# Optimization experiments

Measured on AMD Instinct MI355X. Metric: run time of the kernel, lower is better.

Reference implementation:

```python
import jax, jax.numpy as jnp
import numpy as np

N, E, F, H, D, B = 50000, 800000, 128, 4, 32, 8  # nodes, edges, feat, heads, head_dim, graphs
NEG_SLOPE = 0.2


def _layer_norm(x, g, b, eps=1e-5):
    mu = jnp.mean(x, axis=-1, keepdims=True)
    var = jnp.var(x, axis=-1, keepdims=True)
    return (x - mu) * jax.lax.rsqrt(var + eps) * g + b


def _gat(x, src, dst, W, a_src, a_dst, bias):
    # PyG GATConv (eval): linear -> per-node alpha terms -> edge logits ->
    # per-destination segment softmax -> scatter-add weighted messages.
    h = (x @ W).reshape(N, H, D)                                  # [N,H,D]
    al_s = jnp.einsum('nhd,hd->nh', h, a_src)                     # [N,H]
    al_d = jnp.einsum('nhd,hd->nh', h, a_dst)                     # [N,H]
    logits = jax.nn.leaky_relu(al_s[src] + al_d[dst], NEG_SLOPE)  # [E+N,H]
    m = jax.ops.segment_max(logits, dst, num_segments=N)          # [N,H]
    ex = jnp.exp(logits - m[dst])
    denom = jax.ops.segment_sum(ex, dst, num_segments=N)          # [N,H]
    alpha = ex / denom[dst]                                       # [E+N,H]
    msg = h[src] * alpha[..., None]                               # [E+N,H,D]
    out = jax.ops.segment_sum(msg, dst, num_segments=N)           # [N,H,D]
    return out.reshape(N, H * D) + bias


def _gat_block(x, src, dst, W, a_src, a_dst, bias, ln_g, ln_b):
    out = _gat(x, src, dst, W, a_src, a_dst, bias)
    return _layer_norm(out + x, ln_g, ln_b)  # residual: dims match (128==128)


def setup_inputs() -> dict:
    key = jax.random.key(0)
    ks = jax.random.split(key, 24)
    s = 0.05
    inp = {
        'x': jax.random.normal(ks[0], (N, F), jnp.float32),
        'edge_index': jax.random.randint(ks[1], (2, E), 0, N, jnp.int32),
        'batch': jnp.sort(jax.random.randint(ks[2], (N,), 0, B, jnp.int32)),
    }
    i = 3
    for p in ('loc', 'reg'):
        inp[p + '_W'] = jax.random.normal(ks[i], (F, H * D)) * s; i += 1
        inp[p + '_att_src'] = jax.random.normal(ks[i], (H, D)) * s; i += 1
        inp[p + '_att_dst'] = jax.random.normal(ks[i], (H, D)) * s; i += 1
        inp[p + '_bias'] = jnp.zeros((H * D,))
        inp[p + '_ln_g'] = jnp.ones((F,))
        inp[p + '_ln_b'] = jnp.zeros((F,))
    inp['gp_W1'] = jax.random.normal(ks[i], (F, F)) * s; i += 1
    inp['gp_b1'] = jnp.zeros((F,))
    inp['gp_W2'] = jax.random.normal(ks[i], (F, F)) * s; i += 1
    inp['gp_b2'] = jnp.zeros((F,))
    inp['fu_W1'] = jax.random.normal(ks[i], (3 * F, 2 * F)) * s; i += 1
    inp['fu_b1'] = jnp.zeros((2 * F,))
    inp['fu_W2'] = jax.random.normal(ks[i], (2 * F, F)) * s; i += 1
    inp['fu_b2'] = jnp.zeros((F,))
    inp['fu_ln_g'] = jnp.ones((F,))
    inp['fu_ln_b'] = jnp.zeros((F,))
    return inp


def reference(x, edge_index, batch,
              loc_W, loc_att_src, loc_att_dst, loc_bias, loc_ln_g, loc_ln_b,
              reg_W, reg_att_src, reg_att_dst, reg_bias, reg_ln_g, reg_ln_b,
              gp_W1, gp_b1, gp_W2, gp_b2,
              fu_W1, fu_b1, fu_W2, fu_b2, fu_ln_g, fu_ln_b):
    # add self-loops (PyG GATConv default add_self_loops=True)
    loops = jnp.arange(N, dtype=edge_index.dtype)
    src = jnp.concatenate([edge_index[0], loops])
    dst = jnp.concatenate([edge_index[1], loops])

    local = _gat_block(x, src, dst, loc_W, loc_att_src, loc_att_dst, loc_bias, loc_ln_g, loc_ln_b)
    regional = _gat_block(x, src, dst, reg_W, reg_att_src, reg_att_dst, reg_bias, reg_ln_g, reg_ln_b)

    # global mean pool per graph, broadcast back to nodes
    sums = jax.ops.segment_sum(x, batch, num_segments=B)                  # [B,F]
    cnts = jax.ops.segment_sum(jnp.ones((N, 1), x.dtype), batch, num_segments=B)
    gctx = (sums / cnts)[batch]                                           # [N,F]
    gfeat = jax.nn.relu(gctx @ gp_W1 + gp_b1) @ gp_W2 + gp_b2

    cat = jnp.concatenate([local, regional, gfeat], axis=-1)              # [N,3F]
    fused = jax.nn.relu(cat @ fu_W1 + fu_b1) @ fu_W2 + fu_b2
    return _layer_norm(fused, fu_ln_g, fu_ln_b)
```

## Files before the change

kernel.cpp:

```cpp
#include <hip/hip_runtime.h>

#define NN 50000
#define EE 800000
#define FF 128
#define HH 4
#define BB 8
#define NEG 0.2f
#define NBLK ((NN + 255) / 256)

typedef __attribute__((ext_vector_type(8))) short s8v;
typedef __attribute__((ext_vector_type(4))) float f4v;

__device__ __forceinline__ unsigned short f2b(float f) {
    union { float f; unsigned u; } v; v.f = f;
    unsigned r = v.u + 0x7fffu + ((v.u >> 16) & 1u);
    return (unsigned short)(r >> 16);
}
__device__ __forceinline__ float b2f(unsigned short h) {
    union { unsigned u; float f; } v; v.u = ((unsigned)h) << 16;
    return v.f;
}
__device__ __forceinline__ float uasf(unsigned u) {
    union { unsigned u; float f; } v; v.u = u; return v.f;
}
__device__ __forceinline__ float lrelu(float t) { return t > 0.f ? t : NEG * t; }

__global__ void k_init(int* cur, float* pooled) {
    int i = blockIdx.x * 256 + threadIdx.x;
    if (i < NN) cur[i] = 1;
    if (i < BB * FF) pooled[i] = 0.f;
}

__global__ void k_count(const int* __restrict__ ei, int* cur) {
    int i = blockIdx.x * 256 + threadIdx.x;
    if (i < EE) atomicAdd(&cur[ei[EE + i]], 1);
}

__global__ __launch_bounds__(256) void k_scanA(int* cur, int* row_ptr, int* bsum) {
    __shared__ int wsum[4];
    int b = blockIdx.x, t = threadIdx.x;
    int i = b * 256 + t;
    int v = (i < NN) ? cur[i] : 0;
    if (i < NN) cur[i] = 0;
    int lane = t & 63, w = t >> 6;
    int sc = v;
#pragma unroll
    for (int off = 1; off < 64; off <<= 1) {
        int n = __shfl_up(sc, off);
        if (lane >= off) sc += n;
    }
    if (lane == 63) wsum[w] = sc;
    __syncthreads();
    int woff = 0;
    for (int k = 0; k < w; k++) woff += wsum[k];
    int incl = sc + woff;
    if (i < NN) row_ptr[i + 1] = incl;
    if (t == 255) bsum[b] = incl;
    if (i == 0) row_ptr[0] = 0;
}

__global__ __launch_bounds__(256) void k_scanB(const int* __restrict__ bsum, int* boff) {
    __shared__ int wsum[4];
    int t = threadIdx.x;
    int v = (t < NBLK) ? bsum[t] : 0;
    int lane = t & 63, w = t >> 6;
    int sc = v;
#pragma unroll
    for (int off = 1; off < 64; off <<= 1) {
        int n = __shfl_up(sc, off);
        if (lane >= off) sc += n;
    }
    if (lane == 63) wsum[w] = sc;
    __syncthreads();
    int woff = 0;
    for (int k = 0; k < w; k++) woff += wsum[k];
    if (t < NBLK) boff[t] = sc + woff - v;
}

__global__ __launch_bounds__(256) void k_scanC(int* row_ptr, const int* __restrict__ boff) {
    int i = blockIdx.x * 256 + threadIdx.x;
    if (i < NN) row_ptr[i + 1] += boff[blockIdx.x];
}

__global__ void k_scatter(const int* __restrict__ ei, const int* __restrict__ row_ptr,
                          int* cur, int* col) {
    int i = blockIdx.x * 256 + threadIdx.x;
    if (i < EE) {
        int s = ei[i], d = ei[EE + i];
        int p = atomicAdd(&cur[d], 1);
        col[row_ptr[d] + p] = s;
    } else if (i < EE + NN) {
        int n = i - EE;
        int p = atomicAdd(&cur[n], 1);
        col[row_ptr[n] + p] = n;
    }
}

__global__ void k_convw(const float* __restrict__ locW, const float* __restrict__ regW,
                        const float* __restrict__ W1, const float* __restrict__ W2,
                        unsigned short* __restrict__ Wt, unsigned short* __restrict__ W1t,
                        unsigned short* __restrict__ W2t) {
    int i = blockIdx.x * 256 + threadIdx.x;
    if (i < 32768) {
        int n = i >> 7, k = i & 127;
        float v = n < 128 ? locW[k * 128 + n] : regW[k * 128 + n - 128];
        Wt[i] = f2b(v);
    } else if (i < 32768 + 98304) {
        int j = i - 32768; int n = j / 384, k = j - n * 384;
        W1t[j] = f2b(W1[k * 256 + n]);
    } else if (i < 163840) {
        int j = i - 131072; int n = j >> 8, k = j & 255;
        W2t[j] = f2b(W2[k * 128 + n]);
    }
}

__global__ __launch_bounds__(256) void k_gemm1(
    const float* __restrict__ x,
    const unsigned short* __restrict__ Wt,
    const float* __restrict__ loc_as, const float* __restrict__ loc_ad,
    const float* __restrict__ reg_as, const float* __restrict__ reg_ad,
    unsigned* __restrict__ hc,
    float* __restrict__ als_l, float* __restrict__ ald_l,
    float* __restrict__ als_r, float* __restrict__ ald_r) {
    __shared__ unsigned short As[4 * 64 * 8];
    __shared__ unsigned short Bs[4 * 256 * 8];
    __shared__ unsigned short Hs[32 * 64 * 8];
    int t = threadIdx.x;
    int w = t >> 6, l = t & 63;
    int lq = l >> 4, lr = l & 15;
    int r0 = blockIdx.x * 64;

    int srow = t >> 2, sg = t & 3;
    int snode = r0 + srow; if (snode >= NN) snode = NN - 1;
    const float* xrow = x + (size_t)snode * 128 + sg * 8;

    f4v acc[4][4];
#pragma unroll
    for (int a0 = 0; a0 < 4; a0++)
#pragma unroll
        for (int b0 = 0; b0 < 4; b0++) acc[a0][b0] = (f4v){0.f, 0.f, 0.f, 0.f};

    for (int ks = 0; ks < 4; ++ks) {
        {
            float4 f0 = *(const float4*)(xrow + ks * 32);
            float4 f1 = *(const float4*)(xrow + ks * 32 + 4);
            unsigned short u[8] = { f2b(f0.x), f2b(f0.y), f2b(f0.z), f2b(f0.w),
                                    f2b(f1.x), f2b(f1.y), f2b(f1.z), f2b(f1.w) };
            *(s8v*)&As[(sg * 64 + srow) * 8] = *(const s8v*)u;
        }
#pragma unroll
        for (int it = 0; it < 4; ++it) {
            int c = t + it * 256;
            int g = c & 3, n = c >> 2;
            *(s8v*)&Bs[(g * 256 + n) * 8] = *(const s8v*)&Wt[(size_t)n * 128 + ks * 32 + g * 8];
        }
        __syncthreads();
        s8v af[4], bf[4];
#pragma unroll
        for (int rf = 0; rf < 4; ++rf) af[rf] = *(const s8v*)&As[(lq * 64 + rf * 16 + lr) * 8];
#pragma unroll
        for (int cf = 0; cf < 4; ++cf) bf[cf] = *(const s8v*)&Bs[(lq * 256 + w * 64 + cf * 16 + lr) * 8];
#pragma unroll
        for (int rf = 0; rf < 4; ++rf)
#pragma unroll
            for (int cf = 0; cf < 4; ++cf)
                acc[rf][cf] = __builtin_amdgcn_mfma_f32_16x16x32_bf16(af[rf], bf[cf], acc[rf][cf], 0, 0, 0);
        __syncthreads();
    }
#pragma unroll
    for (int cf = 0; cf < 4; ++cf) {
        int c = w * 64 + cf * 16 + lr;
#pragma unroll
        for (int rf = 0; rf < 4; ++rf)
#pragma unroll
            for (int i = 0; i < 4; ++i) {
                int row = rf * 16 + lq * 4 + i;
                Hs[((c >> 3) * 64 + row) * 8 + (c & 7)] = f2b(acc[rf][cf][i]);
            }
    }
    __syncthreads();
#pragma unroll
    for (int it = 0; it < 16; ++it) {
        int idx = t + it * 256;
        int row = idx >> 6, fp = idx & 63;
        int node = r0 + row;
        if (node < NN) {
            int c0 = 2 * fp;
            int c1 = 128 + 2 * fp;
            unsigned lo = *(const unsigned*)&Hs[((c0 >> 3) * 64 + row) * 8 + (c0 & 7)];
            unsigned hi = *(const unsigned*)&Hs[((c1 >> 3) * 64 + row) * 8 + (c1 & 7)];
            uint2 p; p.x = lo; p.y = hi;
            *(uint2*)&hc[(size_t)node * 128 + fp * 2] = p;
        }
    }
#pragma unroll
    for (int it = 0; it < 4; ++it) {
        int row = it * 16 + (t >> 4);
        int node = r0 + row;
        int q = t & 15;
        int gat = q >> 3, sd = (q >> 2) & 1, head = q & 3;
        const float* av = gat ? (sd ? reg_ad : reg_as) : (sd ? loc_ad : loc_as);
        float s = 0.f;
        int cbase = gat * 128 + head * 32;
        for (int d = 0; d < 32; ++d) {
            int c = cbase + d;
            s += b2f(Hs[((c >> 3) * 64 + row) * 8 + (c & 7)]) * av[head * 32 + d];
        }
        if (node < NN) {
            float* outp = gat ? (sd ? ald_r : als_r) : (sd ? ald_l : als_l);
            outp[(size_t)node * 4 + head] = s;
        }
    }
}

__global__ void k_pool(const float* __restrict__ x, const int* __restrict__ batch,
                       float* pooled) {
    int t = threadIdx.x;
    int f = t & 127, half = t >> 7;
    int rstart = blockIdx.x * 256;
    int rend = rstart + 256; if (rend > NN) rend = NN;
    float acc = 0.f; int cur_b = -1;
    for (int r = rstart + half; r < rend; r += 2) {
        int b = batch[r];
        if (b != cur_b) {
            if (cur_b >= 0) atomicAdd(&pooled[cur_b * 128 + f], acc);
            cur_b = b; acc = 0.f;
        }
        acc += x[r * 128 + f];
    }
    if (cur_b >= 0) atomicAdd(&pooled[cur_b * 128 + f], acc);
}

__global__ __launch_bounds__(256) void k_gfeat8(
    const float* __restrict__ pooled, const int* __restrict__ batch,
    const float* __restrict__ W1, const float* __restrict__ b1,
    const float* __restrict__ W2, const float* __restrict__ b2,
    unsigned short* __restrict__ g8b) {
    __shared__ float mean_s[128];
    __shared__ float hid_s[128];
    __shared__ float part[256];
    __shared__ int bnd[2];
    int b = blockIdx.x, t = threadIdx.x;
    if (t < 2) {
        int target = b + t;
        int lo = 0, hi = NN;
        while (lo < hi) { int mid = (lo + hi) >> 1; if (batch[mid] < target) lo = mid + 1; else hi = mid; }
        bnd[t] = lo;
    }
    __syncthreads();
    int cnt = bnd[1] - bnd[0];
    float inv = cnt ? 1.f / (float)cnt : 0.f;
    if (t < 128) mean_s[t] = pooled[b * 128 + t] * inv;
    __syncthreads();
    int c = t & 127, kh = t >> 7;
    float a = 0.f;
    for (int k = kh * 64; k < kh * 64 + 64; k++) a += mean_s[k] * W1[k * 128 + c];
    part[t] = a;
    __syncthreads();
    if (t < 128) hid_s[t] = fmaxf(part[t] + part[t + 128] + b1[t], 0.f);
    __syncthreads();
    float a2 = 0.f;
    for (int k = kh * 64; k < kh * 64 + 64; k++) a2 += hid_s[k] * W2[k * 128 + c];
    part[t] = a2;
    __syncthreads();
    if (t < 128) g8b[b * 128 + t] = f2b(part[t] + part[t + 128] + b2[t]);
}

__global__ __launch_bounds__(256) void k_gat(
    const int* __restrict__ row_ptr, const int* __restrict__ col,
    const unsigned* __restrict__ hc,
    const float* __restrict__ als_l, const float* __restrict__ ald_l,
    const float* __restrict__ als_r, const float* __restrict__ ald_r,
    const float* __restrict__ x,
    const float* __restrict__ loc_bias, const float* __restrict__ loc_g, const float* __restrict__ loc_b,
    const float* __restrict__ reg_bias, const float* __restrict__ reg_g, const float* __restrict__ reg_b,
    unsigned short* __restrict__ out_local, unsigned short* __restrict__ out_reg) {
    __shared__ float exA[4][64][4];
    __shared__ float exB[4][64][4];
    __shared__ int   colb[4][64];
    __shared__ int   degs[4];
    int w = threadIdx.x >> 6, lane = threadIdx.x & 63;
    int hA = lane >> 4;
    int node = blockIdx.x * 4 + w;
    int rp0 = row_ptr[node];
    int deg = row_ptr[node + 1] - rp0;
    if (lane == 0) degs[w] = deg;
    float4 adL = *(const float4*)&ald_l[(size_t)node * 4];
    float4 adR = *(const float4*)&ald_r[(size_t)node * 4];
    __syncthreads();
    int maxdeg = max(max(degs[0], degs[1]), max(degs[2], degs[3]));
    int chunks = (maxdeg + 63) >> 6;

    float sL0 = 0.f, sL1 = 0.f, sL2 = 0.f, sL3 = 0.f;
    float sR0 = 0.f, sR1 = 0.f, sR2 = 0.f, sR3 = 0.f;
    for (int base = 0; base < deg; base += 64) {
        int i = base + lane;
        bool v = i < deg;
        int s = col[rp0 + (v ? i : deg - 1)];
        float4 aL = *(const float4*)&als_l[(size_t)s * 4];
        float4 aR = *(const float4*)&als_r[(size_t)s * 4];
        float e0 = __expf(lrelu(aL.x + adL.x));
        float e1 = __expf(lrelu(aL.y + adL.y));
        float e2 = __expf(lrelu(aL.z + adL.z));
        float e3 = __expf(lrelu(aL.w + adL.w));
        float f0 = __expf(lrelu(aR.x + adR.x));
        float f1 = __expf(lrelu(aR.y + adR.y));
        float f2 = __expf(lrelu(aR.z + adR.z));
        float f3 = __expf(lrelu(aR.w + adR.w));
        if (!v) { e0 = e1 = e2 = e3 = f0 = f1 = f2 = f3 = 0.f; }
        *(float4*)&exA[w][lane][0] = make_float4(e0, e1, e2, e3);
        *(float4*)&exB[w][lane][0] = make_float4(f0, f1, f2, f3);
        colb[w][lane] = s;
        sL0 += e0; sL1 += e1; sL2 += e2; sL3 += e3;
        sR0 += f0; sR1 += f1; sR2 += f2; sR3 += f3;
    }
    __syncthreads();
#pragma unroll
    for (int off = 32; off; off >>= 1) {
        sL0 += __shfl_xor(sL0, off); sL1 += __shfl_xor(sL1, off);
        sL2 += __shfl_xor(sL2, off); sL3 += __shfl_xor(sL3, off);
        sR0 += __shfl_xor(sR0, off); sR1 += __shfl_xor(sR1, off);
        sR2 += __shfl_xor(sR2, off); sR3 += __shfl_xor(sR3, off);
    }
    float iA = (hA & 2) ? ((hA & 1) ? 1.f / sL3 : 1.f / sL2)
                        : ((hA & 1) ? 1.f / sL1 : 1.f / sL0);
    float iB = (hA & 2) ? ((hA & 1) ? 1.f / sR3 : 1.f / sR2)
                        : ((hA & 1) ? 1.f / sR1 : 1.f / sR0);

    float a0 = 0.f, a1 = 0.f, b0 = 0.f, b1 = 0.f;
    const uint2* hcp = (const uint2*)hc;
    if (chunks == 1) {
#pragma unroll 4
        for (int e = 0; e < deg; ++e) {
            int s = colb[w][e];
            float eAv = exA[w][e][hA];
            float eBv = exB[w][e][hA];
            uint2 u = hcp[(size_t)s * 64 + lane];
            a0 += eAv * uasf(u.x << 16);
            a1 += eAv * uasf(u.x & 0xffff0000u);
            b0 += eBv * uasf(u.y << 16);
            b1 += eBv * uasf(u.y & 0xffff0000u);
        }
    } else {
        for (int c = 0; c < chunks; ++c) {
            int base = c * 64, i = base + lane;
            if (i < deg) {
                int s = col[rp0 + i];
                float4 aL = *(const float4*)&als_l[(size_t)s * 4];
                float4 aR = *(const float4*)&als_r[(size_t)s * 4];
                *(float4*)&exA[w][lane][0] = make_float4(
                    __expf(lrelu(aL.x + adL.x)), __expf(lrelu(aL.y + adL.y)),
                    __expf(lrelu(aL.z + adL.z)), __expf(lrelu(aL.w + adL.w)));
                *(float4*)&exB[w][lane][0] = make_float4(
                    __expf(lrelu(aR.x + adR.x)), __expf(lrelu(aR.y + adR.y)),
                    __expf(lrelu(aR.z + adR.z)), __expf(lrelu(aR.w + adR.w)));
                colb[w][lane] = s;
            }
            __syncthreads();
            int nc = deg - base; nc = nc < 0 ? 0 : (nc > 64 ? 64 : nc);
#pragma unroll 4
            for (int e = 0; e < nc; ++e) {
                int s = colb[w][e];
                float eAv = exA[w][e][hA];
                float eBv = exB[w][e][hA];
                uint2 u = hcp[(size_t)s * 64 + lane];
                a0 += eAv * uasf(u.x << 16);
                a1 += eAv * uasf(u.x & 0xffff0000u);
                b0 += eBv * uasf(u.y << 16);
                b1 += eBv * uasf(u.y & 0xffff0000u);
            }
            __syncthreads();
        }
    }

    int f = 2 * lane;
    float2 xr = *(const float2*)&x[(size_t)node * 128 + f];
    float2 lbi = *(const float2*)&loc_bias[f];
    float2 rbi = *(const float2*)&reg_bias[f];
    float v0 = a0 * iA + lbi.x + xr.x;
    float v1 = a1 * iA + lbi.y + xr.y;
    float u0 = b0 * iB + rbi.x + xr.x;
    float u1 = b1 * iB + rbi.y + xr.y;

    float sv = v0 + v1, su = u0 + u1;
#pragma unroll
    for (int off = 32; off; off >>= 1) { sv += __shfl_xor(sv, off); su += __shfl_xor(su, off); }
    float mv = sv * (1.f / 128.f), mu = su * (1.f / 128.f);
    float dv0 = v0 - mv, dv1 = v1 - mv, du0 = u0 - mu, du1 = u1 - mu;
    float qv = dv0 * dv0 + dv1 * dv1, qu = du0 * du0 + du1 * du1;
#pragma unroll
    for (int off = 32; off; off >>= 1) { qv += __shfl_xor(qv, off); qu += __shfl_xor(qu, off); }
    float rv = rsqrtf(qv * (1.f / 128.f) + 1e-5f), ru = rsqrtf(qu * (1.f / 128.f) + 1e-5f);
    float2 lg = *(const float2*)&loc_g[f], lb2 = *(const float2*)&loc_b[f];
    float2 rg = *(const float2*)&reg_g[f], rb2 = *(const float2*)&reg_b[f];
    unsigned pv = (unsigned)f2b(dv0 * rv * lg.x + lb2.x) | ((unsigned)f2b(dv1 * rv * lg.y + lb2.y) << 16);
    unsigned pu = (unsigned)f2b(du0 * ru * rg.x + rb2.x) | ((unsigned)f2b(du1 * ru * rg.y + rb2.y) << 16);
    *(unsigned*)&out_local[(size_t)node * 128 + f] = pv;
    *(unsigned*)&out_reg[(size_t)node * 128 + f]   = pu;
}

__global__ __launch_bounds__(256) void k_fusedm(
    const unsigned short* __restrict__ localb, const unsigned short* __restrict__ regionalb,
    const unsigned short* __restrict__ g8b, const int* __restrict__ batch,
    const unsigned short* __restrict__ W1t, const float* __restrict__ b1,
    const unsigned short* __restrict__ W2t, const float* __restrict__ b2,
    const float* __restrict__ lng, const float* __restrict__ lnb,
    float* __restrict__ out) {
    __shared__ unsigned short As[4 * 64 * 8];
    __shared__ unsigned short Bs[4 * 256 * 8];
    __shared__ unsigned short Hs[32 * 64 * 8];
    __shared__ unsigned short W2s[4 * 128 * 8];
    int t = threadIdx.x;
    int w = t >> 6, l = t & 63;
    int lq = l >> 4, lr = l & 15;
    int r0 = blockIdx.x * 64;

    int srow = t >> 2, sg = t & 3;
    int snode = r0 + srow; if (snode >= NN) snode = NN - 1;
    int sbatch = batch[snode];

    f4v acc[4][4];
#pragma unroll
    for (int a0 = 0; a0 < 4; a0++)
#pragma unroll
        for (int b0 = 0; b0 < 4; b0++) acc[a0][b0] = (f4v){0.f, 0.f, 0.f, 0.f};

    for (int ks = 0; ks < 12; ++ks) {
        int seg = ks >> 2;
        int ko = (ks & 3) * 32 + sg * 8;
        const unsigned short* src =
            seg == 0 ? localb + (size_t)snode * 128 + ko :
            seg == 1 ? regionalb + (size_t)snode * 128 + ko :
                       g8b + (size_t)sbatch * 128 + ko;
        *(s8v*)&As[(sg * 64 + srow) * 8] = *(const s8v*)src;
#pragma unroll
        for (int it = 0; it < 4; ++it) {
            int c = t + it * 256;
            int g = c & 3, n = c >> 2;
            *(s8v*)&Bs[(g * 256 + n) * 8] = *(const s8v*)&W1t[(size_t)n * 384 + ks * 32 + g * 8];
        }
        __syncthreads();
        s8v af[4], bf[4];
#pragma unroll
        for (int rf = 0; rf < 4; ++rf) af[rf] = *(const s8v*)&As[(lq * 64 + rf * 16 + lr) * 8];
#pragma unroll
        for (int cf = 0; cf < 4; ++cf) bf[cf] = *(const s8v*)&Bs[(lq * 256 + w * 64 + cf * 16 + lr) * 8];
#pragma unroll
        for (int rf = 0; rf < 4; ++rf)
#pragma unroll
            for (int cf = 0; cf < 4; ++cf)
                acc[rf][cf] = __builtin_amdgcn_mfma_f32_16x16x32_bf16(af[rf], bf[cf], acc[rf][cf], 0, 0, 0);
        __syncthreads();
    }
#pragma unroll
    for (int cf = 0; cf < 4; ++cf) {
        int c = w * 64 + cf * 16 + lr;
        float bc = b1[c];
#pragma unroll
        for (int rf = 0; rf < 4; ++rf)
#pragma unroll
            for (int i = 0; i < 4; ++i) {
                int row = rf * 16 + lq * 4 + i;
                float v0 = acc[rf][cf][i] + bc;
                Hs[((c >> 3) * 64 + row) * 8 + (c & 7)] = f2b(v0 > 0.f ? v0 : 0.f);
            }
    }
    __syncthreads();
    f4v a2[8];
#pragma unroll
    for (int cf = 0; cf < 8; ++cf) a2[cf] = (f4v){0.f, 0.f, 0.f, 0.f};
    for (int ks = 0; ks < 8; ++ks) {
#pragma unroll
        for (int it = 0; it < 2; ++it) {
            int c = t + it * 256;
            int g = c & 3, n = c >> 2;
            *(s8v*)&W2s[(g * 128 + n) * 8] = *(const s8v*)&W2t[(size_t)n * 256 + ks * 32 + g * 8];
        }
        __syncthreads();
        s8v af = *(const s8v*)&Hs[((ks * 4 + lq) * 64 + w * 16 + lr) * 8];
#pragma unroll
        for (int cf = 0; cf < 8; ++cf) {
            s8v bfv = *(const s8v*)&W2s[(lq * 128 + cf * 16 + lr) * 8];
            a2[cf] = __builtin_amdgcn_mfma_f32_16x16x32_bf16(af, bfv, a2[cf], 0, 0, 0);
        }
        __syncthreads();
    }
    float b2c[8], gc[8], bc2[8];
#pragma unroll
    for (int cf = 0; cf < 8; ++cf) {
        int c = cf * 16 + lr;
        b2c[cf] = b2[c]; gc[cf] = lng[c]; bc2[cf] = lnb[c];
    }
#pragma unroll
    for (int i = 0; i < 4; ++i) {
        int row = w * 16 + lq * 4 + i;
        int node = r0 + row;
        float vals[8]; float s = 0.f;
#pragma unroll
        for (int cf = 0; cf < 8; ++cf) { vals[cf] = a2[cf][i] + b2c[cf]; s += vals[cf]; }
        s += __shfl_xor(s, 1); s += __shfl_xor(s, 2); s += __shfl_xor(s, 4); s += __shfl_xor(s, 8);
        float mean = s * (1.f / 128.f);
        float vs = 0.f;
#pragma unroll
        for (int cf = 0; cf < 8; ++cf) { float d = vals[cf] - mean; vs += d * d; }
        vs += __shfl_xor(vs, 1); vs += __shfl_xor(vs, 2); vs += __shfl_xor(vs, 4); vs += __shfl_xor(vs, 8);
        float rstd = rsqrtf(vs * (1.f / 128.f) + 1e-5f);
        if (node < NN) {
#pragma unroll
            for (int cf = 0; cf < 8; ++cf)
                out[(size_t)node * 128 + cf * 16 + lr] = (vals[cf] - mean) * rstd * gc[cf] + bc2[cf];
        }
    }
}

extern "C" void kernel_launch(void* const* d_in, const int* in_sizes, int n_in,
                              void* d_out, int out_size, void* d_ws, size_t ws_size,
                              hipStream_t stream) {
    const float* x      = (const float*)d_in[0];
    const int*   ei     = (const int*)d_in[1];
    const int*   batch  = (const int*)d_in[2];
    const float* locW   = (const float*)d_in[3];
    const float* loc_as = (const float*)d_in[4];
    const float* loc_ad = (const float*)d_in[5];
    const float* loc_bi = (const float*)d_in[6];
    const float* loc_g  = (const float*)d_in[7];
    const float* loc_b  = (const float*)d_in[8];
    const float* regW   = (const float*)d_in[9];
    const float* reg_as = (const float*)d_in[10];
    const float* reg_ad = (const float*)d_in[11];
    const float* reg_bi = (const float*)d_in[12];
    const float* reg_g  = (const float*)d_in[13];
    const float* reg_b  = (const float*)d_in[14];
    const float* gp_W1  = (const float*)d_in[15];
    const float* gp_b1  = (const float*)d_in[16];
    const float* gp_W2  = (const float*)d_in[17];
    const float* gp_b2  = (const float*)d_in[18];
    const float* fu_W1  = (const float*)d_in[19];
    const float* fu_b1  = (const float*)d_in[20];
    const float* fu_W2  = (const float*)d_in[21];
    const float* fu_b2  = (const float*)d_in[22];
    const float* fu_lg  = (const float*)d_in[23];
    const float* fu_lb  = (const float*)d_in[24];
    float* out = (float*)d_out;

    char* ws = (char*)d_ws;
    size_t off = 0;
    auto alloc = [&](size_t bytes) { void* p = ws + off; off += (bytes + 255) & ~(size_t)255; return p; };
    unsigned* hc              = (unsigned*)alloc((size_t)NN * 128 * 4);
    unsigned short* localb    = (unsigned short*)alloc((size_t)NN * 128 * 2);
    unsigned short* regionalb = (unsigned short*)alloc((size_t)NN * 128 * 2);
    float* als_l  = (float*)alloc((size_t)NN * 4 * 4);
    float* ald_l  = (float*)alloc((size_t)NN * 4 * 4);
    float* als_r  = (float*)alloc((size_t)NN * 4 * 4);
    float* ald_r  = (float*)alloc((size_t)NN * 4 * 4);
    int* row_ptr  = (int*)alloc((size_t)(NN + 1) * 4);
    int* cur      = (int*)alloc((size_t)NN * 4);
    int* col      = (int*)alloc((size_t)(EE + NN) * 4);
    float* pooled = (float*)alloc((size_t)BB * 128 * 4);
    unsigned short* g8b = (unsigned short*)alloc((size_t)BB * 128 * 2);
    unsigned short* Wt  = (unsigned short*)alloc((size_t)32768 * 2);
    unsigned short* W1t = (unsigned short*)alloc((size_t)98304 * 2);
    unsigned short* W2t = (unsigned short*)alloc((size_t)32768 * 2);
    int* bsum = (int*)alloc((size_t)NBLK * 4);
    int* boff = (int*)alloc((size_t)NBLK * 4);

    hipLaunchKernelGGL(k_init, dim3((NN + 255) / 256), dim3(256), 0, stream, cur, pooled);
    hipLaunchKernelGGL(k_count, dim3((EE + 255) / 256), dim3(256), 0, stream, ei, cur);
    hipLaunchKernelGGL(k_scanA, dim3(NBLK), dim3(256), 0, stream, cur, row_ptr, bsum);
    hipLaunchKernelGGL(k_scanB, dim3(1), dim3(256), 0, stream, bsum, boff);
    hipLaunchKernelGGL(k_scanC, dim3(NBLK), dim3(256), 0, stream, row_ptr, boff);
    hipLaunchKernelGGL(k_scatter, dim3((EE + NN + 255) / 256), dim3(256), 0, stream, ei, row_ptr, cur, col);
    hipLaunchKernelGGL(k_convw, dim3(640), dim3(256), 0, stream,
                       locW, regW, fu_W1, fu_W2, Wt, W1t, W2t);
    hipLaunchKernelGGL(k_gemm1, dim3((NN + 63) / 64), dim3(256), 0, stream,
                       x, Wt, loc_as, loc_ad, reg_as, reg_ad,
                       hc, als_l, ald_l, als_r, ald_r);
    hipLaunchKernelGGL(k_pool, dim3((NN + 255) / 256), dim3(256), 0, stream, x, batch, pooled);
    hipLaunchKernelGGL(k_gfeat8, dim3(BB), dim3(256), 0, stream,
                       pooled, batch, gp_W1, gp_b1, gp_W2, gp_b2, g8b);
    hipLaunchKernelGGL(k_gat, dim3(NN / 4), dim3(256), 0, stream,
                       row_ptr, col, hc, als_l, ald_l, als_r, ald_r, x,
                       loc_bi, loc_g, loc_b, reg_bi, reg_g, reg_b,
                       localb, regionalb);
    hipLaunchKernelGGL(k_fusedm, dim3((NN + 63) / 64), dim3(256), 0, stream,
                       localb, regionalb, g8b, batch,
                       W1t, fu_b1, W2t, fu_b2, fu_lg, fu_lb, out);
}
```

Before: 311.7 us.

## Split GAT aggregation wave into two edge halves with 16-byte gathers, merge init kernels

The GAT aggregation kernel now has each half of a wavefront process alternate edges, with every lane loading a uint4 (4 features for both heads) instead of a uint2. The two halves are combined with a cross-half shuffle before the layer norm, which is now reduced over 32 lanes. The goal is fewer dependent gather iterations per node and wider memory transactions. The weight-conversion kernel is also folded into the init kernel to save one launch. The multi-chunk path gains extra barriers, and all lanes still run the final reductions although only half of them write.

```diff
diff --git a/kernel.cpp b/kernel.cpp
--- a/kernel.cpp
+++ b/kernel.cpp
@@ -25,10 +25,26 @@
 }
 __device__ __forceinline__ float lrelu(float t) { return t > 0.f ? t : NEG * t; }
 
-__global__ void k_init(int* cur, float* pooled) {
+__global__ void k_prep(const float* __restrict__ locW, const float* __restrict__ regW,
+                       const float* __restrict__ W1, const float* __restrict__ W2,
+                       unsigned short* __restrict__ Wt, unsigned short* __restrict__ W1t,
+                       unsigned short* __restrict__ W2t, int* cur, float* pooled) {
     int i = blockIdx.x * 256 + threadIdx.x;
-    if (i < NN) cur[i] = 1;
-    if (i < BB * FF) pooled[i] = 0.f;
+    if (i < 32768) {
+        int n = i >> 7, k = i & 127;
+        float v = n < 128 ? locW[k * 128 + n] : regW[k * 128 + n - 128];
+        Wt[i] = f2b(v);
+    } else if (i < 131072) {
+        int j = i - 32768; int n = j / 384, k = j - n * 384;
+        W1t[j] = f2b(W1[k * 256 + n]);
+    } else if (i < 163840) {
+        int j = i - 131072; int n = j >> 8, k = j & 255;
+        W2t[j] = f2b(W2[k * 128 + n]);
+    } else {
+        int j = i - 163840;
+        if (j < NN) cur[j] = 1;
+        if (j < BB * FF) pooled[j] = 0.f;
+    }
 }
 
 __global__ void k_count(const int* __restrict__ ei, int* cur) {
@@ -93,24 +109,6 @@
         int n = i - EE;
         int p = atomicAdd(&cur[n], 1);
         col[row_ptr[n] + p] = n;
-    }
-}
-
-__global__ void k_convw(const float* __restrict__ locW, const float* __restrict__ regW,
-                        const float* __restrict__ W1, const float* __restrict__ W2,
-                        unsigned short* __restrict__ Wt, unsigned short* __restrict__ W1t,
-                        unsigned short* __restrict__ W2t) {
-    int i = blockIdx.x * 256 + threadIdx.x;
-    if (i < 32768) {
-        int n = i >> 7, k = i & 127;
-        float v = n < 128 ? locW[k * 128 + n] : regW[k * 128 + n - 128];
-        Wt[i] = f2b(v);
-    } else if (i < 32768 + 98304) {
-        int j = i - 32768; int n = j / 384, k = j - n * 384;
-        W1t[j] = f2b(W1[k * 256 + n]);
-    } else if (i < 163840) {
-        int j = i - 131072; int n = j >> 8, k = j & 255;
-        W2t[j] = f2b(W2[k * 128 + n]);
     }
 }
 
@@ -280,7 +278,8 @@
     __shared__ int   colb[4][64];
     __shared__ int   degs[4];
     int w = threadIdx.x >> 6, lane = threadIdx.x & 63;
-    int hA = lane >> 4;
+    int half = lane >> 5, j = lane & 31;
+    int h2 = j >> 3;
     int node = blockIdx.x * 4 + w;
     int rp0 = row_ptr[node];
     int deg = row_ptr[node + 1] - rp0;
@@ -322,81 +321,114 @@
         sR0 += __shfl_xor(sR0, off); sR1 += __shfl_xor(sR1, off);
         sR2 += __shfl_xor(sR2, off); sR3 += __shfl_xor(sR3, off);
     }
-    float iA = (hA & 2) ? ((hA & 1) ? 1.f / sL3 : 1.f / sL2)
-                        : ((hA & 1) ? 1.f / sL1 : 1.f / sL0);
-    float iB = (hA & 2) ? ((hA & 1) ? 1.f / sR3 : 1.f / sR2)
-                        : ((hA & 1) ? 1.f / sR1 : 1.f / sR0);
-
-    float a0 = 0.f, a1 = 0.f, b0 = 0.f, b1 = 0.f;
-    const uint2* hcp = (const uint2*)hc;
+    float iA = (h2 & 2) ? ((h2 & 1) ? 1.f / sL3 : 1.f / sL2)
+                        : ((h2 & 1) ? 1.f / sL1 : 1.f / sL0);
+    float iB = (h2 & 2) ? ((h2 & 1) ? 1.f / sR3 : 1.f / sR2)
+                        : ((h2 & 1) ? 1.f / sR1 : 1.f / sR0);
+
+    float aL0 = 0.f, aL1 = 0.f, aL2 = 0.f, aL3 = 0.f;
+    float bR0 = 0.f, bR1 = 0.f, bR2 = 0.f, bR3 = 0.f;
+    const uint4* hc4 = (const uint4*)hc;
     if (chunks == 1) {
+        int npair = (deg + 1) >> 1;
 #pragma unroll 4
-        for (int e = 0; e < deg; ++e) {
+        for (int it = 0; it < npair; ++it) {
+            int e = 2 * it + half;
             int s = colb[w][e];
-            float eAv = exA[w][e][hA];
-            float eBv = exB[w][e][hA];
-            uint2 u = hcp[(size_t)s * 64 + lane];
-            a0 += eAv * uasf(u.x << 16);
-            a1 += eAv * uasf(u.x & 0xffff0000u);
-            b0 += eBv * uasf(u.y << 16);
-            b1 += eBv * uasf(u.y & 0xffff0000u);
+            float eA = exA[w][e][h2];
+            float eB = exB[w][e][h2];
+            uint4 u = hc4[(size_t)s * 32 + j];
+            aL0 += eA * uasf(u.x << 16);
+            aL1 += eA * uasf(u.x & 0xffff0000u);
+            bR0 += eB * uasf(u.y << 16);
+            bR1 += eB * uasf(u.y & 0xffff0000u);
+            aL2 += eA * uasf(u.z << 16);
+            aL3 += eA * uasf(u.z & 0xffff0000u);
+            bR2 += eB * uasf(u.w << 16);
+            bR3 += eB * uasf(u.w & 0xffff0000u);
         }
     } else {
         for (int c = 0; c < chunks; ++c) {
             int base = c * 64, i = base + lane;
-            if (i < deg) {
-                int s = col[rp0 + i];
-                float4 aL = *(const float4*)&als_l[(size_t)s * 4];
-                float4 aR = *(const float4*)&als_r[(size_t)s * 4];
-                *(float4*)&exA[w][lane][0] = make_float4(
-                    __expf(lrelu(aL.x + adL.x)), __expf(lrelu(aL.y + adL.y)),
-                    __expf(lrelu(aL.z + adL.z)), __expf(lrelu(aL.w + adL.w)));
-                *(float4*)&exB[w][lane][0] = make_float4(
-                    __expf(lrelu(aR.x + adR.x)), __expf(lrelu(aR.y + adR.y)),
-                    __expf(lrelu(aR.z + adR.z)), __expf(lrelu(aR.w + adR.w)));
-                colb[w][lane] = s;
-            }
+            bool v = i < deg;
+            int s0 = col[rp0 + (v ? i : deg - 1)];
+            float4 aL = *(const float4*)&als_l[(size_t)s0 * 4];
+            float4 aR = *(const float4*)&als_r[(size_t)s0 * 4];
+            float e0 = __expf(lrelu(aL.x + adL.x));
+            float e1 = __expf(lrelu(aL.y + adL.y));
+            float e2 = __expf(lrelu(aL.z + adL.z));
+            float e3 = __expf(lrelu(aL.w + adL.w));
+            float f0 = __expf(lrelu(aR.x + adR.x));
+            float f1 = __expf(lrelu(aR.y + adR.y));
+            float f2 = __expf(lrelu(aR.z + adR.z));
+            float f3 = __expf(lrelu(aR.w + adR.w));
+            if (!v) { e0 = e1 = e2 = e3 = f0 = f1 = f2 = f3 = 0.f; }
+            __syncthreads();
+            *(float4*)&exA[w][lane][0] = make_float4(e0, e1, e2, e3);
+            *(float4*)&exB[w][lane][0] = make_float4(f0, f1, f2, f3);
+            colb[w][lane] = s0;
             __syncthreads();
             int nc = deg - base; nc = nc < 0 ? 0 : (nc > 64 ? 64 : nc);
+            int npair = (nc + 1) >> 1;
 #pragma unroll 4
-            for (int e = 0; e < nc; ++e) {
+            for (int it = 0; it < npair; ++it) {
+                int e = 2 * it + half;
                 int s = colb[w][e];
-                float eAv = exA[w][e][hA];
-                float eBv = exB[w][e][hA];
-                uint2 u = hcp[(size_t)s * 64 + lane];
-                a0 += eAv * uasf(u.x << 16);
-                a1 += eAv * uasf(u.x & 0xffff0000u);
-                b0 += eBv * uasf(u.y << 16);
-                b1 += eBv * uasf(u.y & 0xffff0000u);
+                float eA = exA[w][e][h2];
+                float eB = exB[w][e][h2];
+                uint4 u = hc4[(size_t)s * 32 + j];
+                aL0 += eA * uasf(u.x << 16);
+                aL1 += eA * uasf(u.x & 0xffff0000u);
+                bR0 += eB * uasf(u.y << 16);
+                bR1 += eB * uasf(u.y & 0xffff0000u);
+                aL2 += eA * uasf(u.z << 16);
+                aL3 += eA * uasf(u.z & 0xffff0000u);
+                bR2 += eB * uasf(u.w << 16);
+                bR3 += eB * uasf(u.w & 0xffff0000u);
             }
-            __syncthreads();
-        }
-    }
-
-    int f = 2 * lane;
-    float2 xr = *(const float2*)&x[(size_t)node * 128 + f];
-    float2 lbi = *(const float2*)&loc_bias[f];
-    float2 rbi = *(const float2*)&reg_bias[f];
-    float v0 = a0 * iA + lbi.x + xr.x;
-    float v1 = a1 * iA + lbi.y + xr.y;
-    float u0 = b0 * iB + rbi.x + xr.x;
-    float u1 = b1 * iB + rbi.y + xr.y;
-
-    float sv = v0 + v1, su = u0 + u1;
-#pragma unroll
-    for (int off = 32; off; off >>= 1) { sv += __shfl_xor(sv, off); su += __shfl_xor(su, off); }
+        }
+    }
+
+    aL0 += __shfl_xor(aL0, 32); aL1 += __shfl_xor(aL1, 32);
+    aL2 += __shfl_xor(aL2, 32); aL3 += __shfl_xor(aL3, 32);
+    bR0 += __shfl_xor(bR0, 32); bR1 += __shfl_xor(bR1, 32);
+    bR2 += __shfl_xor(bR2, 32); bR3 += __shfl_xor(bR3, 32);
+
+    int f0i = 4 * j;
+    float4 xr  = *(const float4*)&x[(size_t)node * 128 + f0i];
+    float4 lbi = *(const float4*)&loc_bias[f0i];
+    float4 rbi = *(const float4*)&reg_bias[f0i];
+    float v0 = aL0 * iA + lbi.x + xr.x;
+    float v1 = aL1 * iA + lbi.y + xr.y;
+    float v2 = aL2 * iA + lbi.z + xr.z;
+    float v3 = aL3 * iA + lbi.w + xr.w;
+    float u0 = bR0 * iB + rbi.x + xr.x;
+    float u1 = bR1 * iB + rbi.y + xr.y;
+    float u2 = bR2 * iB + rbi.z + xr.z;
+    float u3 = bR3 * iB + rbi.w + xr.w;
+
+    float sv = v0 + v1 + v2 + v3, su = u0 + u1 + u2 + u3;
+#pragma unroll
+    for (int off = 16; off; off >>= 1) { sv += __shfl_xor(sv, off); su += __shfl_xor(su, off); }
     float mv = sv * (1.f / 128.f), mu = su * (1.f / 128.f);
-    float dv0 = v0 - mv, dv1 = v1 - mv, du0 = u0 - mu, du1 = u1 - mu;
-    float qv = dv0 * dv0 + dv1 * dv1, qu = du0 * du0 + du1 * du1;
-#pragma unroll
-    for (int off = 32; off; off >>= 1) { qv += __shfl_xor(qv, off); qu += __shfl_xor(qu, off); }
+    float dv0 = v0 - mv, dv1 = v1 - mv, dv2 = v2 - mv, dv3 = v3 - mv;
+    float du0 = u0 - mu, du1 = u1 - mu, du2 = u2 - mu, du3 = u3 - mu;
+    float qv = dv0 * dv0 + dv1 * dv1 + dv2 * dv2 + dv3 * dv3;
+    float qu = du0 * du0 + du1 * du1 + du2 * du2 + du3 * du3;
+#pragma unroll
+    for (int off = 16; off; off >>= 1) { qv += __shfl_xor(qv, off); qu += __shfl_xor(qu, off); }
     float rv = rsqrtf(qv * (1.f / 128.f) + 1e-5f), ru = rsqrtf(qu * (1.f / 128.f) + 1e-5f);
-    float2 lg = *(const float2*)&loc_g[f], lb2 = *(const float2*)&loc_b[f];
-    float2 rg = *(const float2*)&reg_g[f], rb2 = *(const float2*)&reg_b[f];
-    unsigned pv = (unsigned)f2b(dv0 * rv * lg.x + lb2.x) | ((unsigned)f2b(dv1 * rv * lg.y + lb2.y) << 16);
-    unsigned pu = (unsigned)f2b(du0 * ru * rg.x + rb2.x) | ((unsigned)f2b(du1 * ru * rg.y + rb2.y) << 16);
-    *(unsigned*)&out_local[(size_t)node * 128 + f] = pv;
-    *(unsigned*)&out_reg[(size_t)node * 128 + f]   = pu;
+    if (half == 0) {
+        float4 lg = *(const float4*)&loc_g[f0i], lb2 = *(const float4*)&loc_b[f0i];
+        float4 rg = *(const float4*)&reg_g[f0i], rb2 = *(const float4*)&reg_b[f0i];
+        uint2 pv, pu;
+        pv.x = (unsigned)f2b(dv0 * rv * lg.x + lb2.x) | ((unsigned)f2b(dv1 * rv * lg.y + lb2.y) << 16);
+        pv.y = (unsigned)f2b(dv2 * rv * lg.z + lb2.z) | ((unsigned)f2b(dv3 * rv * lg.w + lb2.w) << 16);
+        pu.x = (unsigned)f2b(du0 * ru * rg.x + rb2.x) | ((unsigned)f2b(du1 * ru * rg.y + rb2.y) << 16);
+        pu.y = (unsigned)f2b(du2 * ru * rg.z + rb2.z) | ((unsigned)f2b(du3 * ru * rg.w + rb2.w) << 16);
+        *(uint2*)&out_local[(size_t)node * 128 + f0i] = pv;
+        *(uint2*)&out_reg[(size_t)node * 128 + f0i]   = pu;
+    }
 }
 
 __global__ __launch_bounds__(256) void k_fusedm(
@@ -564,14 +596,13 @@
     int* bsum = (int*)alloc((size_t)NBLK * 4);
     int* boff = (int*)alloc((size_t)NBLK * 4);
 
-    hipLaunchKernelGGL(k_init, dim3((NN + 255) / 256), dim3(256), 0, stream, cur, pooled);
+    hipLaunchKernelGGL(k_prep, dim3(640 + NBLK), dim3(256), 0, stream,
+                       locW, regW, fu_W1, fu_W2, Wt, W1t, W2t, cur, pooled);
     hipLaunchKernelGGL(k_count, dim3((EE + 255) / 256), dim3(256), 0, stream, ei, cur);
     hipLaunchKernelGGL(k_scanA, dim3(NBLK), dim3(256), 0, stream, cur, row_ptr, bsum);
     hipLaunchKernelGGL(k_scanB, dim3(1), dim3(256), 0, stream, bsum, boff);
     hipLaunchKernelGGL(k_scanC, dim3(NBLK), dim3(256), 0, stream, row_ptr, boff);
     hipLaunchKernelGGL(k_scatter, dim3((EE + NN + 255) / 256), dim3(256), 0, stream, ei, row_ptr, cur, col);
-    hipLaunchKernelGGL(k_convw, dim3(640), dim3(256), 0, stream,
-                       locW, regW, fu_W1, fu_W2, Wt, W1t, W2t);
     hipLaunchKernelGGL(k_gemm1, dim3((NN + 63) / 64), dim3(256), 0, stream,
                        x, Wt, loc_as, loc_ad, reg_as, reg_ad,
                        hc, als_l, ald_l, als_r, ald_r);
```

After: 311.4 us (median of 2 runs). About the same (-0.1%).
